# Kernel optimization log

Hardware: AMD Instinct MI355X
Metric: run time of the kernel (lower is better)

The kernel has to match this reference:

```python
import jax, jax.numpy as jnp
import numpy as np
import math

EPS = 1e-12
SUPPORT = 1  # support_num
NEIGHBOR_NUM = 32

def _l2norm(x, axis):
    n = jnp.sqrt(jnp.sum(x * x, axis=axis, keepdims=True))
    return x / jnp.maximum(n, EPS)

def _sq_dist(a, b):
    # a: (bs, v1, 3), b: (bs, v2, 3) -> (bs, v1, v2)
    inner = jnp.einsum('bic,bjc->bij', a, b)
    a2 = jnp.sum(a * a, axis=-1)
    b2 = jnp.sum(b * b, axis=-1)
    return a2[:, :, None] + b2[:, None, :] - 2.0 * inner

def _knn(verts, k):
    d = _sq_dist(verts, verts)
    _, idx = jax.lax.top_k(-d, k + 1)
    return idx[:, :, 1:]  # drop self

def _gather(t, idx):
    # t: (bs, v, d), idx: (bs, ...) -> (bs, ..., d)
    return jax.vmap(lambda ti, ii: ti[ii])(t, idx)

def _dir_theta(nb_idx, verts, directions):
    nbr = _gather(verts, nb_idx) - verts[:, :, None, :]  # (bs, v, n, 3)
    nbr = _l2norm(nbr, -1)
    sup = _l2norm(directions, 0)  # (3, s*out)
    return jax.nn.relu(jnp.einsum('bvnc,ck->bvnk', nbr, sup))

def _conv_surface(nb_idx, verts, directions, kernel_num):
    theta = _dir_theta(nb_idx, verts, directions)
    bs, v, n, _ = theta.shape
    theta = theta.reshape(bs, v, n, SUPPORT, kernel_num)
    return jnp.sum(jnp.max(theta, axis=2), axis=2)  # (bs, v, kernel)

def _conv_layer(nb_idx, verts, fm, w, b, directions, out_ch):
    theta = _dir_theta(nb_idx, verts, directions)  # (bs, v, n, s*out)
    f = fm @ w + b  # (bs, v, (s+1)*out)
    center = f[..., :out_ch]
    supp_nb = _gather(f[..., out_ch:], nb_idx)  # (bs, v, n, s*out)
    bs, v, n, _ = theta.shape
    act = (theta * supp_nb).reshape(bs, v, n, SUPPORT, out_ch)
    return center + jnp.sum(jnp.max(act, axis=2), axis=2)

def _pool(verts, fm, sample_idx, nbk=4):
    nb = _knn(verts, nbk)
    pooled = jnp.max(_gather(fm, nb), axis=2)
    return verts[:, sample_idx, :], pooled[:, sample_idx, :]

def _nearest(target, source):
    return jnp.argmin(_sq_dist(target, source), axis=-1)  # (bs, v1)

def _forward(vertices, sample_idx1, sample_idx2, dir0, w1, b1, d1, w2, b2, d2,
             w3, b3, d3, w4, b4, d4, cw1, cb1, cw2, cb2, cw3, cb3):
    nb = _knn(vertices, NEIGHBOR_NUM)
    fm_0 = jax.nn.relu(_conv_surface(nb, vertices, dir0, 128))
    fm_1 = jax.nn.relu(_conv_layer(nb, vertices, fm_0, w1, b1, d1, 128))
    v_p1, fm_p1 = _pool(vertices, fm_1, sample_idx1)
    nb = _knn(v_p1, NEIGHBOR_NUM)
    fm_2 = jax.nn.relu(_conv_layer(nb, v_p1, fm_p1, w2, b2, d2, 256))
    fm_3 = jax.nn.relu(_conv_layer(nb, v_p1, fm_2, w3, b3, d3, 256))
    v_p2, fm_p2 = _pool(v_p1, fm_3, sample_idx2)
    nb = _knn(v_p2, NEIGHBOR_NUM)
    fm_4 = _conv_layer(nb, v_p2, fm_p2, w4, b4, d4, 512)  # no relu
    f_global = jnp.max(fm_4, axis=1)  # (bs, 512)
    near1 = _nearest(vertices, v_p1)
    near2 = _nearest(vertices, v_p2)
    fm_2u = _gather(fm_2, near1)
    fm_3u = _gather(fm_3, near1)
    fm_4u = _gather(fm_4, near2)
    bs, v = vertices.shape[0], vertices.shape[1]
    fg = jnp.broadcast_to(f_global[:, None, :], (bs, v, f_global.shape[-1]))
    fuse = jnp.concatenate([fm_0, fm_1, fm_2u, fm_3u, fm_4u, fg], axis=2)  # (bs, v, 1792)
    h = jax.nn.relu(jnp.einsum('bvc,oc->bvo', fuse, cw1) + cb1)
    h = jax.nn.relu(jnp.einsum('bvc,oc->bvo', h, cw2) + cb2)
    return jnp.einsum('bvc,oc->bvo', h, cw3) + cb3  # (bs, v, class_num)


def setup_inputs() -> dict:
    key = jax.random.key(0)
    ks = jax.random.split(key, 24)
    BS, N, CLS = 4, 4096, 13
    def u(k, shape, s):
        return jax.random.uniform(k, shape, jnp.float32, -s, s)
    inp = {}
    inp['vertices'] = jax.random.normal(ks[0], (BS, N, 3), jnp.float32)
    inp['sample_idx1'] = jax.random.permutation(ks[1], N)[:N // 4]
    inp['sample_idx2'] = jax.random.permutation(ks[2], N // 4)[:N // 16]
    inp['dir0'] = u(ks[3], (3, SUPPORT * 128), 1.0 / math.sqrt(SUPPORT * 128))
    def conv_params(k1, k2, k3, cin, cout):
        s = 1.0 / math.sqrt(cout * (SUPPORT + 1))
        return (u(k1, (cin, (SUPPORT + 1) * cout), s),
                u(k2, ((SUPPORT + 1) * cout,), s),
                u(k3, (3, SUPPORT * cout), s))
    inp['w1'], inp['b1'], inp['d1'] = conv_params(ks[4], ks[5], ks[6], 128, 128)
    inp['w2'], inp['b2'], inp['d2'] = conv_params(ks[7], ks[8], ks[9], 128, 256)
    inp['w3'], inp['b3'], inp['d3'] = conv_params(ks[10], ks[11], ks[12], 256, 256)
    inp['w4'], inp['b4'], inp['d4'] = conv_params(ks[13], ks[14], ks[15], 256, 512)
    DF = 1792
    inp['cw1'] = u(ks[16], (512, DF), 1.0 / math.sqrt(DF))
    inp['cb1'] = u(ks[17], (512,), 1.0 / math.sqrt(DF))
    inp['cw2'] = u(ks[18], (512, 512), 1.0 / math.sqrt(512))
    inp['cb2'] = u(ks[19], (512,), 1.0 / math.sqrt(512))
    inp['cw3'] = u(ks[20], (CLS, 512), 1.0 / math.sqrt(512))
    inp['cb3'] = u(ks[21], (CLS,), 1.0 / math.sqrt(512))
    return inp


def reference(vertices, sample_idx1, sample_idx2, dir0, w1, b1, d1, w2, b2, d2,
              w3, b3, d3, w4, b4, d4, cw1, cb1, cw2, cb2, cw3, cb3):
    return _forward(vertices, sample_idx1, sample_idx2, dir0, w1, b1, d1, w2, b2, d2,
                    w3, b3, d3, w4, b4, d4, cw1, cb1, cw2, cb2, cw3, cb3)
```

## Files before the change

### kernel.cpp

```cpp
#include <hip/hip_runtime.h>
#include <cstdint>
#include <cstddef>

namespace {

typedef unsigned short ushort_t;
typedef __bf16 bf16x8 __attribute__((ext_vector_type(8)));
typedef float  f32x4  __attribute__((ext_vector_type(4)));

constexpr int B_ = 4;
constexpr int N0 = 4096;
constexpr int N1 = 1024;
constexpr int N2 = 256;

__device__ __forceinline__ ushort_t f2bf_rne(float x) {
  uint32_t b = __float_as_uint(x);
  b += 0x7FFFu + ((b >> 16) & 1u);
  return (ushort_t)(b >> 16);
}
__device__ __forceinline__ float bf2f(ushort_t h) {
  return __uint_as_float(((uint32_t)h) << 16);
}
__device__ __forceinline__ void split_store(float x, ushort_t* hi, ushort_t* lo,
                                            size_t i) {
  const ushort_t h = f2bf_rne(x);
  hi[i] = h;
  lo[i] = f2bf_rne(x - bf2f(h));
}

__global__ void prep_kernel(
    const float* __restrict__ w1, const float* __restrict__ w2,
    const float* __restrict__ w3, const float* __restrict__ w4,
    const float* __restrict__ cw1, const float* __restrict__ cw2,
    const float* __restrict__ vertices,
    const int* __restrict__ sidx1, const int* __restrict__ sidx2,
    ushort_t* __restrict__ w1th, ushort_t* __restrict__ w1tl,
    ushort_t* __restrict__ w2th, ushort_t* __restrict__ w2tl,
    ushort_t* __restrict__ w3th, ushort_t* __restrict__ w3tl,
    ushort_t* __restrict__ w4th, ushort_t* __restrict__ w4tl,
    ushort_t* __restrict__ w1h, ushort_t* __restrict__ w1l,
    ushort_t* __restrict__ w2h, ushort_t* __restrict__ w2l,
    float* __restrict__ vp1, float* __restrict__ vp2)
{
  const int i = blockIdx.x * blockDim.x + threadIdx.x;
  if (i < 32768) {
    const int j = i, k = j % 128, n = j / 128;
    split_store(w1[(size_t)k * 256 + n], w1th, w1tl, (size_t)n * 128 + k);
  } else if (i < 98304) {
    const int j = i - 32768, k = j % 128, n = j / 128;
    split_store(w2[(size_t)k * 512 + n], w2th, w2tl, (size_t)n * 128 + k);
  } else if (i < 229376) {
    const int j = i - 98304, k = j % 256, n = j / 256;
    split_store(w3[(size_t)k * 512 + n], w3th, w3tl, (size_t)n * 256 + k);
  } else if (i < 491520) {
    const int j = i - 229376, k = j % 256, n = j / 256;
    split_store(w4[(size_t)k * 1024 + n], w4th, w4tl, (size_t)n * 256 + k);
  } else if (i < 1409024) {
    const int j = i - 491520;
    split_store(cw1[j], w1h, w1l, j);
  } else if (i < 1671168) {
    const int j = i - 1409024;
    split_store(cw2[j], w2h, w2l, j);
  } else if (i < 1683456) {
    const int j = i - 1671168;
    const int c = j % 3, q = (j / 3) % N1, b = j / (3 * N1);
    vp1[j] = vertices[((size_t)b * N0 + sidx1[q]) * 3 + c];
  } else if (i < 1686528) {
    const int j = i - 1683456;
    const int c = j % 3, q = (j / 3) % N2, b = j / (3 * N2);
    vp2[j] = vertices[((size_t)b * N0 + sidx1[sidx2[q]]) * 3 + c];
  }
}

__device__ __forceinline__ void bitonic_sort64(float& sd, int& si, int lane) {
#pragma unroll
  for (int kk = 2; kk <= 64; kk <<= 1) {
#pragma unroll
    for (int j = kk >> 1; j > 0; j >>= 1) {
      const float od = __shfl_xor(sd, j);
      const int   oi = __shfl_xor(si, j);
      const bool less    = (sd < od) || (sd == od && si < oi);
      const bool wantMin = ((lane & j) == 0) == ((lane & kk) == 0);
      if (wantMin != less) { sd = od; si = oi; }
    }
  }
}

__device__ __forceinline__ void knn_flush(float& ld, int& li, float& tau,
                                          int cnt, const float* bufd,
                                          const int* bufi, int lane, int Km1) {
  float sd = (lane < cnt) ? bufd[lane] : INFINITY;
  int   si = (lane < cnt) ? bufi[lane] : 0x7fffffff;
  bitonic_sort64(sd, si, lane);
  const float rd = __shfl(sd, 63 - lane);
  const int   ri = __shfl(si, 63 - lane);
  const bool keep = (ld < rd) || (ld == rd && li < ri);
  float md = keep ? ld : rd;
  int   mi = keep ? li : ri;
#pragma unroll
  for (int j = 32; j > 0; j >>= 1) {
    const float od = __shfl_xor(md, j);
    const int   oi = __shfl_xor(mi, j);
    const bool less    = (md < od) || (md == od && mi < oi);
    const bool wantMin = ((lane & j) == 0);
    if (wantMin != less) { md = od; mi = oi; }
  }
  ld = md; li = mi;
  tau = __shfl(ld, Km1);
}

__launch_bounds__(512)
__global__ void knn_mega_kernel(const float* __restrict__ verts,
                                const float* __restrict__ vp1,
                                const float* __restrict__ vp2,
                                int* __restrict__ nb1,
                                int* __restrict__ nb2,
                                int* __restrict__ nb3)
{
  constexpr int K = 32, TILE = 2048;
  __shared__ float4 sp[TILE];
  __shared__ float sbd[8][64];
  __shared__ int   sbi[8][64];

  int bx = blockIdx.x;
  const float* pts; int Q, C; int* out;
  if (bx < 2048)      { pts = verts; Q = N0; C = N0; out = nb1; }
  else if (bx < 2560) { pts = vp1;   Q = N1; C = N1; out = nb2; bx -= 2048; }
  else                { pts = vp2;   Q = N2; C = N2; out = nb3; bx -= 2560; }
  const int bpb = Q / 8;
  const int b  = bx / bpb;
  const int lane = threadIdx.x & 63;
  const int wid  = threadIdx.x >> 6;
  const int q    = (bx % bpb) * 8 + wid;
  const int self = q;
  const float* pb = pts + (size_t)b * C * 3;
  const float qx = pb[self * 3 + 0];
  const float qy = pb[self * 3 + 1];
  const float qz = pb[self * 3 + 2];
  const float q2   = qx * qx + qy * qy + qz * qz;
  const float m2qx = -2.0f * qx, m2qy = -2.0f * qy, m2qz = -2.0f * qz;

  float ld = INFINITY; int li = 0x7fffffff;
  float tau = INFINITY;
  int cnt = 0;
  float* bufd = sbd[wid];
  int*   bufi = sbi[wid];

  auto append = [&](unsigned long long m, bool cand, float d, int ci) {
    const int c = __popcll(m);
    if (cnt + c > 64) {
      knn_flush(ld, li, tau, cnt, bufd, bufi, lane, K - 1);
      cnt = 0;
    }
    const int prefix = __popcll(m & ((1ull << lane) - 1ull));
    if (cand) { bufd[cnt + prefix] = d; bufi[cnt + prefix] = ci; }
    cnt += c;
  };

  for (int t0 = 0; t0 < C; t0 += TILE) {
    const int nt = (C - t0 < TILE) ? (C - t0) : TILE;
    __syncthreads();
    for (int i = threadIdx.x; i < nt; i += 512) {
      const float x = pb[(t0 + i) * 3 + 0];
      const float y = pb[(t0 + i) * 3 + 1];
      const float z = pb[(t0 + i) * 3 + 2];
      sp[i] = make_float4(x, y, z, x * x + y * y + z * z);
    }
    __syncthreads();
    int base = 0;
    if (t0 == 0) {
      const float4 p = sp[lane];
      const float d = fmaf(m2qx, p.x, fmaf(m2qy, p.y, fmaf(m2qz, p.z, p.w + q2)));
      const bool valid = (lane != self);
      float sd = valid ? d : INFINITY;
      int   si = valid ? lane : 0x7fffffff;
      bitonic_sort64(sd, si, lane);
      ld = sd; li = si;
      tau = __shfl(ld, K - 1);
      base = 64;
    }
    for (; base + 128 <= nt; base += 128) {
      const int ci0 = t0 + base + lane;
      const int ci1 = ci0 + 64;
      const float4 p0 = sp[base + lane];
      const float4 p1 = sp[base + 64 + lane];
      const float d0 = fmaf(m2qx, p0.x, fmaf(m2qy, p0.y, fmaf(m2qz, p0.z, p0.w + q2)));
      const float d1 = fmaf(m2qx, p1.x, fmaf(m2qy, p1.y, fmaf(m2qz, p1.z, p1.w + q2)));
      const bool c0 = (ci0 != self) && (d0 < tau);
      const bool c1 = (ci1 != self) && (d1 < tau);
      const unsigned long long m0 = __ballot(c0);
      const unsigned long long m1 = __ballot(c1);
      if (m0) append(m0, c0, d0, ci0);
      if (m1) append(m1, c1, d1, ci1);
    }
    if (base < nt) {
      const int ci = t0 + base + lane;
      const float4 p = sp[base + lane];
      const float d = fmaf(m2qx, p.x, fmaf(m2qy, p.y, fmaf(m2qz, p.z, p.w + q2)));
      const bool c = (ci != self) && (d < tau);
      const unsigned long long m = __ballot(c);
      if (m) append(m, c, d, ci);
    }
  }
  if (cnt > 0) knn_flush(ld, li, tau, cnt, bufd, bufi, lane, K - 1);
  if (lane < K) out[((size_t)b * Q + q) * K + lane] = li;
}

__launch_bounds__(256)
__global__ void nearest_dual_kernel(const float* __restrict__ qpts,
                                    const float* __restrict__ cpts1,
                                    const float* __restrict__ cpts2,
                                    int* __restrict__ out1,
                                    int* __restrict__ out2)
{
  __shared__ float4 sp[1024];
  const int lvl = blockIdx.y;
  const int C = lvl ? N2 : N1;
  const float* cpts = lvl ? cpts2 : cpts1;
  int* out = lvl ? out2 : out1;
  const int lane = threadIdx.x & 63;
  const int wid  = threadIdx.x >> 6;
  const int q    = blockIdx.x * 4 + wid;
  const int b    = q >> 12;
  const float qx = qpts[(size_t)q * 3 + 0];
  const float qy = qpts[(size_t)q * 3 + 1];
  const float qz = qpts[(size_t)q * 3 + 2];
  const float q2   = qx * qx + qy * qy + qz * qz;
  const float m2qx = -2.0f * qx, m2qy = -2.0f * qy, m2qz = -2.0f * qz;
  const float* pb = cpts + (size_t)b * C * 3;

  for (int i = threadIdx.x; i < C; i += 256) {
    const float x = pb[i * 3 + 0];
    const float y = pb[i * 3 + 1];
    const float z = pb[i * 3 + 2];
    sp[i] = make_float4(x, y, z, x * x + y * y + z * z);
  }
  __syncthreads();
  float best = INFINITY; int bi = 0x7fffffff;
  for (int base = 0; base < C; base += 64) {
    const float4 p = sp[base + lane];
    const float d = fmaf(m2qx, p.x, fmaf(m2qy, p.y, fmaf(m2qz, p.z, p.w + q2)));
    if (d < best) { best = d; bi = base + lane; }
  }
#pragma unroll
  for (int j = 1; j < 64; j <<= 1) {
    const float od = __shfl_xor(best, j);
    const int   oi = __shfl_xor(bi, j);
    if (od < best || (od == best && oi < bi)) { best = od; bi = oi; }
  }
  if (lane == 0) out[q] = bi;
}

__global__ void conv_surface_kernel(const float* __restrict__ verts,
                                    const int*   __restrict__ nb,
                                    const float* __restrict__ dir,
                                    int V, int C,
                                    ushort_t* __restrict__ outH,
                                    ushort_t* __restrict__ outL) {
  __shared__ float ux[32], uy[32], uz[32];
  const int bv = blockIdx.x;
  const int b = bv / V;
  const int v = bv - b * V;
  const float* vb = verts + (size_t)b * V * 3;
  if (threadIdx.x < 32) {
    const float cx = vb[v * 3 + 0], cy = vb[v * 3 + 1], cz = vb[v * 3 + 2];
    const int nidx = nb[(size_t)bv * 32 + threadIdx.x];
    const float dx = vb[nidx * 3 + 0] - cx;
    const float dy = vb[nidx * 3 + 1] - cy;
    const float dz = vb[nidx * 3 + 2] - cz;
    const float rn = 1.0f / fmaxf(sqrtf(dx * dx + dy * dy + dz * dz), 1e-12f);
    ux[threadIdx.x] = dx * rn; uy[threadIdx.x] = dy * rn; uz[threadIdx.x] = dz * rn;
  }
  __syncthreads();
  const int o = threadIdx.x;
  float d0 = dir[o], d1 = dir[C + o], d2 = dir[2 * C + o];
  const float rn = 1.0f / fmaxf(sqrtf(d0 * d0 + d1 * d1 + d2 * d2), 1e-12f);
  d0 *= rn; d1 *= rn; d2 *= rn;
  float m = -INFINITY;
#pragma unroll
  for (int n = 0; n < 32; ++n) {
    const float t = fmaxf(0.0f, fmaf(d2, uz[n], fmaf(d1, uy[n], d0 * ux[n])));
    m = fmaxf(m, t);
  }
  split_store(fmaxf(0.0f, m), outH, outL, (size_t)bv * C + o);
}

__global__ void conv_combine_kernel(const float* __restrict__ f,
                                    const int*   __restrict__ nb,
                                    const float* __restrict__ dir,
                                    const float* __restrict__ verts,
                                    int V, int C, int relu,
                                    ushort_t* __restrict__ outH,
                                    ushort_t* __restrict__ outL) {
  __shared__ float ux[32], uy[32], uz[32];
  __shared__ int snb[32];
  const int bv = blockIdx.x;
  const int b = bv / V;
  const int v = bv - b * V;
  const float* vb = verts + (size_t)b * V * 3;
  if (threadIdx.x < 32) {
    const float cx = vb[v * 3 + 0], cy = vb[v * 3 + 1], cz = vb[v * 3 + 2];
    const int nidx = nb[(size_t)bv * 32 + threadIdx.x];
    snb[threadIdx.x] = nidx;
    const float dx = vb[nidx * 3 + 0] - cx;
    const float dy = vb[nidx * 3 + 1] - cy;
    const float dz = vb[nidx * 3 + 2] - cz;
    const float rn = 1.0f / fmaxf(sqrtf(dx * dx + dy * dy + dz * dz), 1e-12f);
    ux[threadIdx.x] = dx * rn; uy[threadIdx.x] = dy * rn; uz[threadIdx.x] = dz * rn;
  }
  __syncthreads();
  const int o = threadIdx.x;
  float d0 = dir[o], d1 = dir[C + o], d2 = dir[2 * C + o];
  const float rn = 1.0f / fmaxf(sqrtf(d0 * d0 + d1 * d1 + d2 * d2), 1e-12f);
  d0 *= rn; d1 *= rn; d2 *= rn;
  const float* fb = f + (size_t)b * V * 2 * C;
  float m = -INFINITY;
#pragma unroll 8
  for (int n = 0; n < 32; ++n) {
    const float t = fmaxf(0.0f, fmaf(d2, uz[n], fmaf(d1, uy[n], d0 * ux[n])));
    const float s = fb[(size_t)snb[n] * 2 * C + C + o];
    m = fmaxf(m, t * s);
  }
  float r = fb[(size_t)v * 2 * C + o] + m;
  if (relu) r = fmaxf(r, 0.0f);
  split_store(r, outH, outL, (size_t)bv * C + o);
}

__global__ void pool_kernel(const ushort_t* __restrict__ fmH,
                            const ushort_t* __restrict__ fmL,
                            const int*   __restrict__ nb,
                            const int*   __restrict__ sidx,
                            int Q, int Vsrc, int C,
                            ushort_t* __restrict__ outH,
                            ushort_t* __restrict__ outL) {
  const int i = blockIdx.x * blockDim.x + threadIdx.x;
  if (i >= B_ * Q * C) return;
  const int c = i % C;
  const int q = (i / C) % Q;
  const int b = i / (C * Q);
  const int* nn = nb + ((size_t)b * Vsrc + sidx[q]) * 32;
  const size_t fb = (size_t)b * Vsrc * C;
  float m = -INFINITY;
#pragma unroll
  for (int t = 0; t < 4; ++t) {
    const size_t idx = fb + (size_t)nn[t] * C + c;
    m = fmaxf(m, bf2f(fmH[idx]) + bf2f(fmL[idx]));
  }
  split_store(m, outH, outL, (size_t)i);
}

__global__ void global_max_kernel(const ushort_t* __restrict__ fmH,
                                  const ushort_t* __restrict__ fmL,
                                  ushort_t* __restrict__ outH,
                                  ushort_t* __restrict__ outL) {
  __shared__ float red[4][64];
  const int t = threadIdx.x;
  const int cl = t & 63, slice = t >> 6;
  const int c = (blockIdx.x & 7) * 64 + cl;
  const int b = blockIdx.x >> 3;
  const size_t base = (size_t)b * 256 * 512 + c;
  float m = -INFINITY;
  for (int v = slice; v < 256; v += 4) {
    const size_t idx = base + (size_t)v * 512;
    m = fmaxf(m, bf2f(fmH[idx]) + bf2f(fmL[idx]));
  }
  red[slice][cl] = m;
  __syncthreads();
  if (slice == 0) {
    m = fmaxf(fmaxf(red[0][cl], red[1][cl]), fmaxf(red[2][cl], red[3][cl]));
    split_store(m, outH, outL, (size_t)b * 512 + c);
  }
}

constexpr int LDT = 36;

template<bool FUSE, bool SPLITOUT, bool RELU>
__launch_bounds__(256)
__global__ void mfma_gemm_kernel(
    const ushort_t* __restrict__ Ahi, const ushort_t* __restrict__ Alo,
    const ushort_t* __restrict__ f0h, const ushort_t* __restrict__ f0l,
    const ushort_t* __restrict__ f1h, const ushort_t* __restrict__ f1l,
    const ushort_t* __restrict__ f2h, const ushort_t* __restrict__ f2l,
    const ushort_t* __restrict__ f3h, const ushort_t* __restrict__ f3l,
    const ushort_t* __restrict__ f4h, const ushort_t* __restrict__ f4l,
    const ushort_t* __restrict__ fgh, const ushort_t* __restrict__ fgl,
    const int* __restrict__ near1, const int* __restrict__ near2,
    const ushort_t* __restrict__ Bhi, const ushort_t* __restrict__ Blo,
    const float* __restrict__ bias, int K,
    float* __restrict__ outF, ushort_t* __restrict__ outHi,
    ushort_t* __restrict__ outLo, int Nn)
{
  __shared__ ushort_t As_h[128 * LDT];
  __shared__ ushort_t As_l[128 * LDT];
  __shared__ ushort_t Bs_h[128 * LDT];
  __shared__ ushort_t Bs_l[128 * LDT];

  const int tid  = threadIdx.x;
  const int lane = tid & 63;
  const int wv   = tid >> 6;
  const int wr   = wv >> 1, wc = wv & 1;
  const int quad = lane >> 4, ml = lane & 15;
  const int m0 = blockIdx.y * 128, n0 = blockIdx.x * 128;

  const int r  = tid >> 1;
  const int hh = (tid & 1) * 16;

  int fb = 0, r1 = 0, r2 = 0;
  if (FUSE) {
    const int m = m0 + r;
    fb = m >> 12;
    r1 = near1[m];
    r2 = near2[m];
  }

  uint4 a0h, a1h, a0l, a1l, b0h, b1h, b0l, b1l;
  auto load_slice = [&](int k0) {
    const int k = k0 + hh;
    {
      const ushort_t *sh, *sl; size_t off;
      if (FUSE) {
        const int m = m0 + r;
        if (k < 128)       { sh = f0h; sl = f0l; off = (size_t)m * 128 + k; }
        else if (k < 256)  { sh = f1h; sl = f1l; off = (size_t)m * 128 + (k - 128); }
        else if (k < 512)  { sh = f2h; sl = f2l; off = ((size_t)fb * 1024 + r1) * 256 + (k - 256); }
        else if (k < 768)  { sh = f3h; sl = f3l; off = ((size_t)fb * 1024 + r1) * 256 + (k - 512); }
        else if (k < 1280) { sh = f4h; sl = f4l; off = ((size_t)fb * 256 + r2) * 512 + (k - 768); }
        else               { sh = fgh; sl = fgl; off = (size_t)fb * 512 + (k - 1280); }
      } else {
        sh = Ahi; sl = Alo; off = (size_t)(m0 + r) * K + k;
      }
      a0h = *(const uint4*)(sh + off); a1h = *(const uint4*)(sh + off + 8);
      a0l = *(const uint4*)(sl + off); a1l = *(const uint4*)(sl + off + 8);
    }
    {
      const size_t off = (size_t)(n0 + r) * K + k;
      b0h = *(const uint4*)(Bhi + off); b1h = *(const uint4*)(Bhi + off + 8);
      b0l = *(const uint4*)(Blo + off); b1l = *(const uint4*)(Blo + off + 8);
    }
  };

  f32x4 acc[4][4];
#pragma unroll
  for (int i = 0; i < 4; ++i)
#pragma unroll
    for (int j = 0; j < 4; ++j) acc[i][j] = f32x4{0.f, 0.f, 0.f, 0.f};

  load_slice(0);
  for (int k0 = 0; k0 < K; k0 += 32) {
    __syncthreads();
    *(uint4*)&As_h[r * LDT + hh]     = a0h;
    *(uint4*)&As_h[r * LDT + hh + 8] = a1h;
    *(uint4*)&As_l[r * LDT + hh]     = a0l;
    *(uint4*)&As_l[r * LDT + hh + 8] = a1l;
    *(uint4*)&Bs_h[r * LDT + hh]     = b0h;
    *(uint4*)&Bs_h[r * LDT + hh + 8] = b1h;
    *(uint4*)&Bs_l[r * LDT + hh]     = b0l;
    *(uint4*)&Bs_l[r * LDT + hh + 8] = b1l;
    __syncthreads();
    if (k0 + 32 < K) load_slice(k0 + 32);

    bf16x8 ah[4], al[4], bh[4], bl[4];
#pragma unroll
    for (int i = 0; i < 4; ++i) {
      const int row = wr * 64 + i * 16 + ml;
      ah[i] = *(const bf16x8*)&As_h[row * LDT + quad * 8];
      al[i] = *(const bf16x8*)&As_l[row * LDT + quad * 8];
    }
#pragma unroll
    for (int j = 0; j < 4; ++j) {
      const int row = wc * 64 + j * 16 + ml;
      bh[j] = *(const bf16x8*)&Bs_h[row * LDT + quad * 8];
      bl[j] = *(const bf16x8*)&Bs_l[row * LDT + quad * 8];
    }
#pragma unroll
    for (int i = 0; i < 4; ++i)
#pragma unroll
      for (int j = 0; j < 4; ++j) {
        acc[i][j] = __builtin_amdgcn_mfma_f32_16x16x32_bf16(al[i], bh[j], acc[i][j], 0, 0, 0);
        acc[i][j] = __builtin_amdgcn_mfma_f32_16x16x32_bf16(ah[i], bl[j], acc[i][j], 0, 0, 0);
        acc[i][j] = __builtin_amdgcn_mfma_f32_16x16x32_bf16(ah[i], bh[j], acc[i][j], 0, 0, 0);
      }
  }

#pragma unroll
  for (int i = 0; i < 4; ++i)
#pragma unroll
    for (int j = 0; j < 4; ++j) {
      const int n = n0 + wc * 64 + j * 16 + ml;
      const float bv = bias[n];
#pragma unroll
      for (int reg = 0; reg < 4; ++reg) {
        const int m = m0 + wr * 64 + i * 16 + quad * 4 + reg;
        float r = acc[i][j][reg] + bv;
        if (RELU) r = fmaxf(r, 0.0f);
        if (SPLITOUT) {
          const ushort_t h = f2bf_rne(r);
          outHi[(size_t)m * Nn + n] = h;
          outLo[(size_t)m * Nn + n] = f2bf_rne(r - bf2f(h));
        } else {
          outF[(size_t)m * Nn + n] = r;
        }
      }
    }
}

__launch_bounds__(256)
__global__ void head_wave_kernel(const float* __restrict__ h,
                                 const float* __restrict__ cw,
                                 const float* __restrict__ cb,
                                 float* __restrict__ out) {
  __shared__ float ws[13 * 512];
  __shared__ float cbs[13];
  const int lane = threadIdx.x & 63;
  const int wid  = threadIdx.x >> 6;
  for (int i = threadIdx.x; i < 13 * 512; i += 256) ws[i] = cw[i];
  if (threadIdx.x < 13) cbs[threadIdx.x] = cb[threadIdx.x];
  __syncthreads();
  const int row = blockIdx.x * 4 + wid;
  const float4* hr = (const float4*)(h + (size_t)row * 512);
  const float4 a0 = hr[lane * 2], a1 = hr[lane * 2 + 1];
#pragma unroll
  for (int o = 0; o < 13; ++o) {
    const float4* wr = (const float4*)(ws + o * 512);
    const float4 w0 = wr[lane * 2], w1 = wr[lane * 2 + 1];
    float p = a0.x * w0.x + a0.y * w0.y + a0.z * w0.z + a0.w * w0.w
            + a1.x * w1.x + a1.y * w1.y + a1.z * w1.z + a1.w * w1.w;
#pragma unroll
    for (int j = 1; j < 64; j <<= 1) p += __shfl_xor(p, j);
    if (lane == 0) out[(size_t)row * 13 + o] = p + cbs[o];
  }
}

}

extern "C" void kernel_launch(void* const* d_in, const int* in_sizes, int n_in,
                              void* d_out, int out_size, void* d_ws, size_t ws_size,
                              hipStream_t stream)
{
  const float* vertices = (const float*)d_in[0];
  const int*   sidx1    = (const int*)  d_in[1];
  const int*   sidx2    = (const int*)  d_in[2];
  const float* dir0     = (const float*)d_in[3];
  const float* w1 = (const float*)d_in[4];
  const float* b1 = (const float*)d_in[5];
  const float* d1 = (const float*)d_in[6];
  const float* w2 = (const float*)d_in[7];
  const float* b2 = (const float*)d_in[8];
  const float* d2 = (const float*)d_in[9];
  const float* w3 = (const float*)d_in[10];
  const float* b3 = (const float*)d_in[11];
  const float* d3 = (const float*)d_in[12];
  const float* w4 = (const float*)d_in[13];
  const float* b4 = (const float*)d_in[14];
  const float* d4 = (const float*)d_in[15];
  const float* cw1 = (const float*)d_in[16];
  const float* cb1 = (const float*)d_in[17];
  const float* cw2 = (const float*)d_in[18];
  const float* cb2 = (const float*)d_in[19];
  const float* cw3 = (const float*)d_in[20];
  const float* cb3 = (const float*)d_in[21];
  (void)in_sizes; (void)n_in; (void)out_size; (void)ws_size;

  char* ws = (char*)d_ws;
  size_t off = 0;
  auto alloc = [&](size_t bytes) -> void* {
    void* p = ws + off;
    off += (bytes + 255) & ~(size_t)255;
    return p;
  };

  int*   nb1   = (int*)  alloc((size_t)B_ * N0 * 32 * 4);
  int*   nb2   = (int*)  alloc((size_t)B_ * N1 * 32 * 4);
  int*   nb3   = (int*)  alloc((size_t)B_ * N2 * 32 * 4);
  float* vp1   = (float*)alloc((size_t)B_ * N1 * 3 * 4);
  float* vp2   = (float*)alloc((size_t)B_ * N2 * 3 * 4);
  int*   near1 = (int*)  alloc((size_t)B_ * N0 * 4);
  int*   near2 = (int*)  alloc((size_t)B_ * N0 * 4);
  float* h2    = (float*)alloc((size_t)B_ * N0 * 512 * 4);
  float* fbuf  = (float*)alloc((size_t)B_ * N0 * 256 * 4);

  const size_t nF0 = (size_t)B_ * N0 * 128;
  const size_t nP1 = (size_t)B_ * N1 * 128;
  const size_t nF2 = (size_t)B_ * N1 * 256;
  const size_t nP2 = (size_t)B_ * N2 * 256;
  const size_t nF4 = (size_t)B_ * N2 * 512;
  const size_t nFg = (size_t)B_ * 512;
  const size_t nW1 = (size_t)512 * 1792;
  const size_t nW2 = (size_t)512 * 512;
  const size_t nH1 = (size_t)B_ * N0 * 512;
  ushort_t* f0h = (ushort_t*)alloc(nF0 * 2); ushort_t* f0l = (ushort_t*)alloc(nF0 * 2);
  ushort_t* f1h = (ushort_t*)alloc(nF0 * 2); ushort_t* f1l = (ushort_t*)alloc(nF0 * 2);
  ushort_t* p1h = (ushort_t*)alloc(nP1 * 2); ushort_t* p1l = (ushort_t*)alloc(nP1 * 2);
  ushort_t* f2h = (ushort_t*)alloc(nF2 * 2); ushort_t* f2l = (ushort_t*)alloc(nF2 * 2);
  ushort_t* f3h = (ushort_t*)alloc(nF2 * 2); ushort_t* f3l = (ushort_t*)alloc(nF2 * 2);
  ushort_t* p2h = (ushort_t*)alloc(nP2 * 2); ushort_t* p2l = (ushort_t*)alloc(nP2 * 2);
  ushort_t* f4h = (ushort_t*)alloc(nF4 * 2); ushort_t* f4l = (ushort_t*)alloc(nF4 * 2);
  ushort_t* fgh = (ushort_t*)alloc(nFg * 2); ushort_t* fgl = (ushort_t*)alloc(nFg * 2);
  ushort_t* w1h = (ushort_t*)alloc(nW1 * 2); ushort_t* w1l = (ushort_t*)alloc(nW1 * 2);
  ushort_t* w2h = (ushort_t*)alloc(nW2 * 2); ushort_t* w2l = (ushort_t*)alloc(nW2 * 2);
  ushort_t* h1h = (ushort_t*)alloc(nH1 * 2); ushort_t* h1l = (ushort_t*)alloc(nH1 * 2);
  ushort_t* w1th = (ushort_t*)alloc((size_t)256 * 128 * 2);
  ushort_t* w1tl = (ushort_t*)alloc((size_t)256 * 128 * 2);
  ushort_t* w2th = (ushort_t*)alloc((size_t)512 * 128 * 2);
  ushort_t* w2tl = (ushort_t*)alloc((size_t)512 * 128 * 2);
  ushort_t* w3th = (ushort_t*)alloc((size_t)512 * 256 * 2);
  ushort_t* w3tl = (ushort_t*)alloc((size_t)512 * 256 * 2);
  ushort_t* w4th = (ushort_t*)alloc((size_t)1024 * 256 * 2);
  ushort_t* w4tl = (ushort_t*)alloc((size_t)1024 * 256 * 2);

  const dim3 blk256(256), blk512(512);
  auto mgemm = [&](const ushort_t* Ah, const ushort_t* Al,
                   const ushort_t* Bh, const ushort_t* Bl, const float* bias,
                   int M, int Nn, int K, float* outF) {
    const dim3 grid(Nn / 128, M / 128);
    mfma_gemm_kernel<false, false, false><<<grid, blk256, 0, stream>>>(
        Ah, Al, nullptr, nullptr, nullptr, nullptr, nullptr, nullptr, nullptr,
        nullptr, nullptr, nullptr, nullptr, nullptr, nullptr, nullptr,
        Bh, Bl, bias, K, outF, nullptr, nullptr, Nn);
  };

  prep_kernel<<<dim3(6588), blk256, 0, stream>>>(
      w1, w2, w3, w4, cw1, cw2, vertices, sidx1, sidx2,
      w1th, w1tl, w2th, w2tl, w3th, w3tl, w4th, w4tl,
      w1h, w1l, w2h, w2l, vp1, vp2);

  knn_mega_kernel<<<dim3(2688), blk512, 0, stream>>>(
      vertices, vp1, vp2, nb1, nb2, nb3);

  conv_surface_kernel<<<dim3(B_ * N0), dim3(128), 0, stream>>>(
      vertices, nb1, dir0, N0, 128, f0h, f0l);
  mgemm(f0h, f0l, w1th, w1tl, b1, B_ * N0, 256, 128, fbuf);
  conv_combine_kernel<<<dim3(B_ * N0), dim3(128), 0, stream>>>(
      fbuf, nb1, d1, vertices, N0, 128, 1, f1h, f1l);

  pool_kernel<<<dim3((B_ * N1 * 128 + 255) / 256), blk256, 0, stream>>>(
      f1h, f1l, nb1, sidx1, N1, N0, 128, p1h, p1l);

  mgemm(p1h, p1l, w2th, w2tl, b2, B_ * N1, 512, 128, fbuf);
  conv_combine_kernel<<<dim3(B_ * N1), dim3(256), 0, stream>>>(
      fbuf, nb2, d2, vp1, N1, 256, 1, f2h, f2l);
  mgemm(f2h, f2l, w3th, w3tl, b3, B_ * N1, 512, 256, fbuf);
  conv_combine_kernel<<<dim3(B_ * N1), dim3(256), 0, stream>>>(
      fbuf, nb2, d3, vp1, N1, 256, 1, f3h, f3l);

  pool_kernel<<<dim3((B_ * N2 * 256 + 255) / 256), blk256, 0, stream>>>(
      f3h, f3l, nb2, sidx2, N2, N1, 256, p2h, p2l);

  mgemm(p2h, p2l, w4th, w4tl, b4, B_ * N2, 1024, 256, fbuf);
  conv_combine_kernel<<<dim3(B_ * N2), dim3(512), 0, stream>>>(
      fbuf, nb3, d4, vp2, N2, 512, 0, f4h, f4l);
  global_max_kernel<<<dim3(B_ * 8), blk256, 0, stream>>>(f4h, f4l, fgh, fgl);

  nearest_dual_kernel<<<dim3((B_ * N0) / 4, 2), blk256, 0, stream>>>(
      vertices, vp1, vp2, near1, near2);

  mfma_gemm_kernel<true, true, true><<<dim3(512 / 128, (B_ * N0) / 128), blk256, 0, stream>>>(
      nullptr, nullptr,
      f0h, f0l, f1h, f1l, f2h, f2l, f3h, f3l, f4h, f4l, fgh, fgl,
      near1, near2, w1h, w1l, cb1, 1792, nullptr, h1h, h1l, 512);
  mfma_gemm_kernel<false, false, true><<<dim3(512 / 128, (B_ * N0) / 128), blk256, 0, stream>>>(
      h1h, h1l,
      nullptr, nullptr, nullptr, nullptr, nullptr, nullptr, nullptr, nullptr,
      nullptr, nullptr, nullptr, nullptr,
      nullptr, nullptr, w2h, w2l, cb2, 512, h2, nullptr, nullptr, 512);
  head_wave_kernel<<<dim3((B_ * N0) / 4), blk256, 0, stream>>>(
      h2, cw3, cb3, (float*)d_out);
}
```

Before: 581.9 us.

## Fuse conv_surface and nearest-neighbor search into the KNN mega kernel

Folds the level-0 surface convolution into the tail of the KNN kernel, so each wave computes its surface features directly from the neighbor indices it holds in registers, using shuffles in place of shared memory and a second nb1 read. The nearest-sample search is also moved into the same launch as extra blocks with 8 queries each. Together these remove two kernel launches and let the independent nearest work overlap with KNN. The cost is more register pressure and a larger 512-thread block for the small nearest work, and the nearest blocks still reserve the big KNN shared array, which may limit occupancy.

```diff
diff --git a/kernel.cpp b/kernel.cpp
--- a/kernel.cpp
+++ b/kernel.cpp
@@ -110,12 +110,17 @@
 }
 
 __launch_bounds__(512)
-__global__ void knn_mega_kernel(const float* __restrict__ verts,
-                                const float* __restrict__ vp1,
-                                const float* __restrict__ vp2,
-                                int* __restrict__ nb1,
-                                int* __restrict__ nb2,
-                                int* __restrict__ nb3)
+__global__ void mega_kernel(const float* __restrict__ verts,
+                            const float* __restrict__ vp1,
+                            const float* __restrict__ vp2,
+                            const float* __restrict__ dir,
+                            int* __restrict__ nb1,
+                            int* __restrict__ nb2,
+                            int* __restrict__ nb3,
+                            ushort_t* __restrict__ f0h,
+                            ushort_t* __restrict__ f0l,
+                            int* __restrict__ near1,
+                            int* __restrict__ near2)
 {
   constexpr int K = 32, TILE = 2048;
   __shared__ float4 sp[TILE];
@@ -123,14 +128,53 @@
   __shared__ int   sbi[8][64];
 
   int bx = blockIdx.x;
-  const float* pts; int Q, C; int* out;
-  if (bx < 2048)      { pts = verts; Q = N0; C = N0; out = nb1; }
+  const int lane = threadIdx.x & 63;
+  const int wid  = threadIdx.x >> 6;
+
+  if (bx >= 2688) {
+    const int seg = bx - 2688;
+    const int lvl = seg >> 11;
+    const int sb  = seg & 2047;
+    const int C   = lvl ? N2 : N1;
+    const float* cpts = lvl ? vp2 : vp1;
+    int* out = lvl ? near2 : near1;
+    const int q = sb * 8 + wid;
+    const int b = q >> 12;
+    const float qx = verts[(size_t)q * 3 + 0];
+    const float qy = verts[(size_t)q * 3 + 1];
+    const float qz = verts[(size_t)q * 3 + 2];
+    const float q2   = qx * qx + qy * qy + qz * qz;
+    const float m2qx = -2.0f * qx, m2qy = -2.0f * qy, m2qz = -2.0f * qz;
+    const float* pb = cpts + (size_t)b * C * 3;
+    for (int i = threadIdx.x; i < C; i += 512) {
+      const float x = pb[i * 3 + 0];
+      const float y = pb[i * 3 + 1];
+      const float z = pb[i * 3 + 2];
+      sp[i] = make_float4(x, y, z, x * x + y * y + z * z);
+    }
+    __syncthreads();
+    float best = INFINITY; int bi = 0x7fffffff;
+    for (int base = 0; base < C; base += 64) {
+      const float4 p = sp[base + lane];
+      const float d = fmaf(m2qx, p.x, fmaf(m2qy, p.y, fmaf(m2qz, p.z, p.w + q2)));
+      if (d < best) { best = d; bi = base + lane; }
+    }
+#pragma unroll
+    for (int j = 1; j < 64; j <<= 1) {
+      const float od = __shfl_xor(best, j);
+      const int   oi = __shfl_xor(bi, j);
+      if (od < best || (od == best && oi < bi)) { best = od; bi = oi; }
+    }
+    if (lane == 0) out[q] = bi;
+    return;
+  }
+
+  const float* pts; int Q, C; int* out; bool isL0 = false;
+  if (bx < 2048)      { pts = verts; Q = N0; C = N0; out = nb1; isL0 = true; }
   else if (bx < 2560) { pts = vp1;   Q = N1; C = N1; out = nb2; bx -= 2048; }
   else                { pts = vp2;   Q = N2; C = N2; out = nb3; bx -= 2560; }
   const int bpb = Q / 8;
   const int b  = bx / bpb;
-  const int lane = threadIdx.x & 63;
-  const int wid  = threadIdx.x >> 6;
   const int q    = (bx % bpb) * 8 + wid;
   const int self = q;
   const float* pb = pts + (size_t)b * C * 3;
@@ -204,85 +248,37 @@
   }
   if (cnt > 0) knn_flush(ld, li, tau, cnt, bufd, bufi, lane, K - 1);
   if (lane < K) out[((size_t)b * Q + q) * K + lane] = li;
-}
-
-__launch_bounds__(256)
-__global__ void nearest_dual_kernel(const float* __restrict__ qpts,
-                                    const float* __restrict__ cpts1,
-                                    const float* __restrict__ cpts2,
-                                    int* __restrict__ out1,
-                                    int* __restrict__ out2)
-{
-  __shared__ float4 sp[1024];
-  const int lvl = blockIdx.y;
-  const int C = lvl ? N2 : N1;
-  const float* cpts = lvl ? cpts2 : cpts1;
-  int* out = lvl ? out2 : out1;
-  const int lane = threadIdx.x & 63;
-  const int wid  = threadIdx.x >> 6;
-  const int q    = blockIdx.x * 4 + wid;
-  const int b    = q >> 12;
-  const float qx = qpts[(size_t)q * 3 + 0];
-  const float qy = qpts[(size_t)q * 3 + 1];
-  const float qz = qpts[(size_t)q * 3 + 2];
-  const float q2   = qx * qx + qy * qy + qz * qz;
-  const float m2qx = -2.0f * qx, m2qy = -2.0f * qy, m2qz = -2.0f * qz;
-  const float* pb = cpts + (size_t)b * C * 3;
-
-  for (int i = threadIdx.x; i < C; i += 256) {
-    const float x = pb[i * 3 + 0];
-    const float y = pb[i * 3 + 1];
-    const float z = pb[i * 3 + 2];
-    sp[i] = make_float4(x, y, z, x * x + y * y + z * z);
-  }
-  __syncthreads();
-  float best = INFINITY; int bi = 0x7fffffff;
-  for (int base = 0; base < C; base += 64) {
-    const float4 p = sp[base + lane];
-    const float d = fmaf(m2qx, p.x, fmaf(m2qy, p.y, fmaf(m2qz, p.z, p.w + q2)));
-    if (d < best) { best = d; bi = base + lane; }
-  }
-#pragma unroll
-  for (int j = 1; j < 64; j <<= 1) {
-    const float od = __shfl_xor(best, j);
-    const int   oi = __shfl_xor(bi, j);
-    if (od < best || (od == best && oi < bi)) { best = od; bi = oi; }
-  }
-  if (lane == 0) out[q] = bi;
-}
-
-__global__ void conv_surface_kernel(const float* __restrict__ verts,
-                                    const int*   __restrict__ nb,
-                                    const float* __restrict__ dir,
-                                    int V, int C,
-                                    ushort_t* __restrict__ outH,
-                                    ushort_t* __restrict__ outL) {
-  __shared__ float ux[32], uy[32], uz[32];
-  const int bv = blockIdx.x;
-  const int b = bv / V;
-  const int v = bv - b * V;
-  const float* vb = verts + (size_t)b * V * 3;
-  if (threadIdx.x < 32) {
-    const float cx = vb[v * 3 + 0], cy = vb[v * 3 + 1], cz = vb[v * 3 + 2];
-    const int nidx = nb[(size_t)bv * 32 + threadIdx.x];
-    const float dx = vb[nidx * 3 + 0] - cx;
-    const float dy = vb[nidx * 3 + 1] - cy;
-    const float dz = vb[nidx * 3 + 2] - cz;
-    const float rn = 1.0f / fmaxf(sqrtf(dx * dx + dy * dy + dz * dz), 1e-12f);
-    ux[threadIdx.x] = dx * rn; uy[threadIdx.x] = dy * rn; uz[threadIdx.x] = dz * rn;
-  }
-  __syncthreads();
-  const int o = threadIdx.x;
-  float d0 = dir[o], d1 = dir[C + o], d2 = dir[2 * C + o];
-  const float rn = 1.0f / fmaxf(sqrtf(d0 * d0 + d1 * d1 + d2 * d2), 1e-12f);
-  d0 *= rn; d1 *= rn; d2 *= rn;
-  float m = -INFINITY;
-#pragma unroll
-  for (int n = 0; n < 32; ++n) {
-    const float t = fmaxf(0.0f, fmaf(d2, uz[n], fmaf(d1, uy[n], d0 * ux[n])));
-    m = fmaxf(m, t);
-  }
-  split_store(fmaxf(0.0f, m), outH, outL, (size_t)bv * C + o);
+
+  if (isL0) {
+    float ux = 0.f, uy = 0.f, uz = 0.f;
+    if (lane < 32) {
+      const float dx = pb[li * 3 + 0] - qx;
+      const float dy = pb[li * 3 + 1] - qy;
+      const float dz = pb[li * 3 + 2] - qz;
+      const float rn = 1.0f / fmaxf(sqrtf(dx * dx + dy * dy + dz * dz), 1e-12f);
+      ux = dx * rn; uy = dy * rn; uz = dz * rn;
+    }
+    const int o1 = lane, o2 = lane + 64;
+    float d0a = dir[o1], d1a = dir[128 + o1], d2a = dir[256 + o1];
+    const float rna = 1.0f / fmaxf(sqrtf(d0a*d0a + d1a*d1a + d2a*d2a), 1e-12f);
+    d0a *= rna; d1a *= rna; d2a *= rna;
+    float d0b = dir[o2], d1b = dir[128 + o2], d2b = dir[256 + o2];
+    const float rnb = 1.0f / fmaxf(sqrtf(d0b*d0b + d1b*d1b + d2b*d2b), 1e-12f);
+    d0b *= rnb; d1b *= rnb; d2b *= rnb;
+    float ma = -INFINITY, mb = -INFINITY;
+#pragma unroll 8
+    for (int n = 0; n < 32; ++n) {
+      const float nx = __shfl(ux, n);
+      const float ny = __shfl(uy, n);
+      const float nz = __shfl(uz, n);
+      const float ta = fmaxf(0.0f, fmaf(d2a, nz, fmaf(d1a, ny, d0a * nx)));
+      const float tb = fmaxf(0.0f, fmaf(d2b, nz, fmaf(d1b, ny, d0b * nx)));
+      ma = fmaxf(ma, ta); mb = fmaxf(mb, tb);
+    }
+    const size_t baseo = ((size_t)b * N0 + q) * 128;
+    split_store(fmaxf(0.0f, ma), f0h, f0l, baseo + o1);
+    split_store(fmaxf(0.0f, mb), f0h, f0l, baseo + o2);
+  }
 }
 
 __global__ void conv_combine_kernel(const float* __restrict__ f,
@@ -624,11 +620,9 @@
       w1th, w1tl, w2th, w2tl, w3th, w3tl, w4th, w4tl,
       w1h, w1l, w2h, w2l, vp1, vp2);
 
-  knn_mega_kernel<<<dim3(2688), blk512, 0, stream>>>(
-      vertices, vp1, vp2, nb1, nb2, nb3);
-
-  conv_surface_kernel<<<dim3(B_ * N0), dim3(128), 0, stream>>>(
-      vertices, nb1, dir0, N0, 128, f0h, f0l);
+  mega_kernel<<<dim3(6784), blk512, 0, stream>>>(
+      vertices, vp1, vp2, dir0, nb1, nb2, nb3, f0h, f0l, near1, near2);
+
   mgemm(f0h, f0l, w1th, w1tl, b1, B_ * N0, 256, 128, fbuf);
   conv_combine_kernel<<<dim3(B_ * N0), dim3(128), 0, stream>>>(
       fbuf, nb1, d1, vertices, N0, 128, 1, f1h, f1l);
@@ -650,9 +644,6 @@
   conv_combine_kernel<<<dim3(B_ * N2), dim3(512), 0, stream>>>(
       fbuf, nb3, d4, vp2, N2, 512, 0, f4h, f4l);
   global_max_kernel<<<dim3(B_ * 8), blk256, 0, stream>>>(f4h, f4l, fgh, fgl);
-
-  nearest_dual_kernel<<<dim3((B_ * N0) / 4, 2), blk256, 0, stream>>>(
-      vertices, vp1, vp2, near1, near2);
 
   mfma_gemm_kernel<true, true, true><<<dim3(512 / 128, (B_ * N0) / 128), blk256, 0, stream>>>(
       nullptr, nullptr,
```

After: 580.7 us. Within noise of the previous version (-0.2%).
